# Kernel optimization log

Hardware: AMD Instinct MI355X
Metric: run time of the kernel (lower is better)

Reference implementation:

```python
import jax, jax.numpy as jnp
import numpy as np

B, S, D, H, HD = 1, 4096, 1024, 16, 64
HALF = HD // 2


def setup_inputs() -> dict:
    key = jax.random.key(0)
    ks = jax.random.split(key, 8)
    std = 0.02
    x = jax.random.normal(ks[0], (B, S, D), dtype=jnp.float32)
    wq_w = jax.random.normal(ks[1], (D, D), dtype=jnp.float32) * std
    wk_w = jax.random.normal(ks[2], (D, D), dtype=jnp.float32) * std
    wv_w = jax.random.normal(ks[3], (D, D), dtype=jnp.float32) * std
    wo_w = jax.random.normal(ks[4], (D, D), dtype=jnp.float32) * std
    wq_b = jnp.zeros((D,), jnp.float32)
    wk_b = jnp.zeros((D,), jnp.float32)
    wv_b = jnp.zeros((D,), jnp.float32)
    wo_b = jnp.zeros((D,), jnp.float32)
    # LLaMA-style rotary frequencies: theta = 10000^{-2i/HD}
    inv_freq = 1.0 / (10000.0 ** (jnp.arange(0, HD, 2, dtype=jnp.float32) / HD))  # [HALF]
    t = jnp.arange(S, dtype=jnp.float32)
    angles = jnp.outer(t, inv_freq)  # [S, HALF]
    freqs_cos = jnp.cos(angles)
    freqs_sin = jnp.sin(angles)
    # causal additive mask (finite large-negative to stay grad-safe)
    mask = jnp.triu(jnp.full((S, S), -1e9, dtype=jnp.float32), k=1)[None, None]
    return {
        "x": x, "start_pos": 0, "freqs_cos": freqs_cos, "freqs_sin": freqs_sin,
        "mask": mask,
        "wq_w": wq_w, "wq_b": wq_b, "wk_w": wk_w, "wk_b": wk_b,
        "wv_w": wv_w, "wv_b": wv_b, "wo_w": wo_w, "wo_b": wo_b,
    }


def _apply_rope(t, cos, sin):
    # t: [B, S, H, HD]; cos/sin: [S, HALF]. Complex multiply on consecutive pairs.
    b, s, h, hd = t.shape
    t2 = t.reshape(b, s, h, hd // 2, 2)
    x0, x1 = t2[..., 0], t2[..., 1]
    c = cos[None, :, None, :]
    sn = sin[None, :, None, :]
    o0 = x0 * c - x1 * sn
    o1 = x0 * sn + x1 * c
    return jnp.stack([o0, o1], axis=-1).reshape(b, s, h, hd)


def reference(x, start_pos, freqs_cos, freqs_sin, mask,
              wq_w, wq_b, wk_w, wk_b, wv_w, wv_b, wo_w, wo_b):
    bsz, seqlen, dim = x.shape
    q = (x @ wq_w.T + wq_b).reshape(bsz, seqlen, H, HD)
    k = (x @ wk_w.T + wk_b).reshape(bsz, seqlen, H, HD)
    v = (x @ wv_w.T + wv_b).reshape(bsz, seqlen, H, HD)
    q = _apply_rope(q, freqs_cos, freqs_sin)
    k = _apply_rope(k, freqs_cos, freqs_sin)
    # [B, H, S, HD]
    q = q.transpose(0, 2, 1, 3)
    k = k.transpose(0, 2, 1, 3)
    v = v.transpose(0, 2, 1, 3)
    scores = jnp.einsum('bhqd,bhkd->bhqk', q, k) / jnp.sqrt(jnp.float32(HD))
    scores = scores + mask
    probs = jax.nn.softmax(scores.astype(jnp.float32), axis=-1).astype(q.dtype)
    out = jnp.einsum('bhqk,bhkd->bhqd', probs, v)  # [B, H, S, HD]
    out = out.transpose(0, 2, 1, 3).reshape(bsz, seqlen, dim)
    return out @ wo_w.T + wo_b
```

## Files before the change

### kernel.cpp

```cpp
#include <hip/hip_runtime.h>


#define S_LEN 4096
#define DIM   1024
#define NH    16
#define HD    64

typedef __attribute__((ext_vector_type(8))) short bf16x8;
typedef __attribute__((ext_vector_type(4))) float f32x4;

__device__ __forceinline__ unsigned short f2b(float f) {
  union { float f; unsigned int u; } v; v.f = f;
  unsigned int r = (v.u + 0x7fffu + ((v.u >> 16) & 1u)) >> 16;
  return (unsigned short)r;
}
__device__ __forceinline__ float b2f(unsigned short h) {
  union { unsigned int u; float f; } v; v.u = ((unsigned int)h) << 16;
  return v.f;
}
__device__ __forceinline__ unsigned int pk2t(float a, float b) {
  union { float f; unsigned int u; } x, y; x.f = a; y.f = b;
  return (x.u >> 16) | (y.u & 0xffff0000u);
}
__device__ __forceinline__ void gload16(const void* g, void* l) {
  __builtin_amdgcn_global_load_lds(
      (const __attribute__((address_space(1))) unsigned int*)g,
      (__attribute__((address_space(3))) unsigned int*)l, 16, 0, 0);
}
__device__ __forceinline__ f32x4 fzero4() { f32x4 z = {0.f, 0.f, 0.f, 0.f}; return z; }

__global__ void cvt_all(const float* __restrict__ x, const float* __restrict__ wq,
                        const float* __restrict__ wk, const float* __restrict__ wv,
                        const float* __restrict__ wo, const float* __restrict__ qb,
                        const float* __restrict__ kb, const float* __restrict__ vbs,
                        const float* __restrict__ ob, unsigned short* __restrict__ xb,
                        unsigned short* __restrict__ wqkvb, unsigned short* __restrict__ wobb,
                        float* __restrict__ biasq, float* __restrict__ biaso) {
  int i = blockIdx.x * 256 + threadIdx.x;
  if (i < 2097152) {
    const float* src; unsigned short* dst; int off;
    if (i < 1048576)      { src = x;  dst = xb;              off = i; }
    else if (i < 1310720) { src = wq; dst = wqkvb;           off = i - 1048576; }
    else if (i < 1572864) { src = wk; dst = wqkvb + 1048576; off = i - 1310720; }
    else if (i < 1835008) { src = wv; dst = wqkvb + 2097152; off = i - 1572864; }
    else                  { src = wo; dst = wobb;            off = i - 1835008; }
    float4 v = ((const float4*)src)[off];
    unsigned int lo = (unsigned int)f2b(v.x) | ((unsigned int)f2b(v.y) << 16);
    unsigned int hi = (unsigned int)f2b(v.z) | ((unsigned int)f2b(v.w) << 16);
    ((uint2*)dst)[off] = make_uint2(lo, hi);
  } else if (i < 2097152 + 1024) {
    int j = i - 2097152;
    if (j < 256)      ((float4*)biasq)[j]              = ((const float4*)qb)[j];
    else if (j < 512) ((float4*)(biasq + 1024))[j-256] = ((const float4*)kb)[j-256];
    else if (j < 768) ((float4*)(biasq + 2048))[j-512] = ((const float4*)vbs)[j-512];
    else              ((float4*)biaso)[j-768]          = ((const float4*)ob)[j-768];
  }
}

__global__ __launch_bounds__(256) void gemm_nt(
    const unsigned short* __restrict__ A, const unsigned short* __restrict__ B,
    const float* __restrict__ bias, float* __restrict__ outF,
    unsigned short* __restrict__ dq, unsigned short* __restrict__ dk,
    unsigned short* __restrict__ vtout, const float* __restrict__ fc,
    const float* __restrict__ fs, int M, int N, int K, int mode) {
  __shared__ alignas(16) unsigned short sA[2][128 * 32];
  __shared__ alignas(16) unsigned short sB[2][128 * 32];
  const int tid = threadIdx.x;
  const int lane = tid & 63, wave = tid >> 6;
  const int ln = lane & 15, quad = lane >> 4;
  const int bm = blockIdx.x * 128, bn = blockIdx.y * 128;
  const int wr = (wave >> 1) * 64, wc = (wave & 1) * 64;

  f32x4 acc[4][4];
#pragma unroll
  for (int i = 0; i < 4; ++i)
#pragma unroll
    for (int j = 0; j < 4; ++j) acc[i][j] = fzero4();

#pragma unroll
  for (int i = 0; i < 2; ++i) {
    int o = (i * 256 + tid) * 16;
    int e = o >> 1;
    int row = e >> 5, col = e & 31;
    gload16(A + (size_t)(bm + row) * K + col, (char*)sA[0] + o);
    gload16(B + (size_t)(bn + row) * K + col, (char*)sB[0] + o);
  }

  int buf = 0;
  for (int k0 = 0; k0 < K; k0 += 32, buf ^= 1) {
    __syncthreads();
    if (k0 + 32 < K) {
#pragma unroll
      for (int i = 0; i < 2; ++i) {
        int o = (i * 256 + tid) * 16;
        int e = o >> 1;
        int row = e >> 5, col = e & 31;
        gload16(A + (size_t)(bm + row) * K + k0 + 32 + col, (char*)sA[buf ^ 1] + o);
        gload16(B + (size_t)(bn + row) * K + k0 + 32 + col, (char*)sB[buf ^ 1] + o);
      }
    }
    bf16x8 af[4], bfr[4];
#pragma unroll
    for (int i = 0; i < 4; ++i) {
      af[i]  = *(const bf16x8*)&sA[buf][(wr + i * 16 + ln) * 32 + quad * 8];
      bfr[i] = *(const bf16x8*)&sB[buf][(wc + i * 16 + ln) * 32 + quad * 8];
    }
#pragma unroll
    for (int i = 0; i < 4; ++i)
#pragma unroll
      for (int j = 0; j < 4; ++j)
        acc[i][j] = __builtin_amdgcn_mfma_f32_16x16x32_bf16(af[i], bfr[j], acc[i][j], 0, 0, 0);
  }

  if (mode == 1) {
#pragma unroll
    for (int i = 0; i < 4; ++i)
#pragma unroll
      for (int j = 0; j < 4; ++j) {
        int n = bn + wc + j * 16 + ln;
        float bi = bias[n];
#pragma unroll
        for (int r = 0; r < 4; ++r) {
          int m = bm + wr + i * 16 + quad * 4 + r;
          outF[(size_t)m * N + n] = acc[i][j][r] + bi;
        }
      }
  } else {
    const int bufi = bn >> 10;
    const int hq = ((bn & 1023) + wc) >> 6;
    if (bufi < 2) {
      unsigned short* const base = bufi == 0 ? dq : dk;
      const float qsc = bufi == 0 ? 0.180336880f : 1.0f;
#pragma unroll
      for (int i = 0; i < 4; ++i)
#pragma unroll
        for (int j = 0; j < 4; ++j) {
          int n = bn + wc + j * 16 + ln;
          float bi = bias[n];
          int hd = j * 16 + ln;
          int pi = hd >> 1;
          bool evn = (ln & 1) == 0;
#pragma unroll
          for (int r = 0; r < 4; ++r) {
            int m = bm + wr + i * 16 + quad * 4 + r;
            float val = acc[i][j][r] + bi;
            float par = __shfl_xor(val, 1);
            float c = fc[m * 32 + pi], sn = fs[m * 32 + pi];
            float o = evn ? (val * c - par * sn) : (par * sn + val * c);
            base[((size_t)(hq * S_LEN + m)) * HD + hd] = f2b(o * qsc);
          }
        }
    } else {
      __syncthreads();
      unsigned short* scr =
          (wave < 2 ? (unsigned short*)sA : (unsigned short*)sB) + (wave & 1) * 4096;
#pragma unroll
      for (int i = 0; i < 4; ++i)
#pragma unroll
        for (int j = 0; j < 4; ++j) {
          int n = bn + wc + j * 16 + ln;
          float bi = bias[n];
          int hd = j * 16 + ln;
#pragma unroll
          for (int r = 0; r < 4; ++r) {
            int sl = i * 16 + quad * 4 + r;
            int byte = hd * 128 + ((((sl >> 3) ^ (hd & 7)) << 4)) + (sl & 7) * 2;
            *(unsigned short*)((char*)scr + byte) = f2b(acc[i][j][r] + bi);
          }
        }
#pragma unroll
      for (int pass = 0; pass < 4; ++pass) {
        int row = pass * 16 + ln;
        uint4 d0 = *(uint4*)((char*)scr + row * 128 + (((quad * 2) ^ (row & 7)) << 4));
        uint4 d1 = *(uint4*)((char*)scr + row * 128 + (((quad * 2 + 1) ^ (row & 7)) << 4));
        uint4* dst = (uint4*)(vtout + ((size_t)(hq * HD + row)) * S_LEN + bm + wr + quad * 16);
        dst[0] = d0;
        dst[1] = d1;
      }
    }
  }
}

__device__ __forceinline__ bf16x8 lds_swzK(const unsigned short* s, int row, int chunk) {
  int byte = row * 128 + ((chunk ^ ((row >> 2) & 7)) << 4);
  return *(const bf16x8*)((const char*)s + byte);
}
__device__ __forceinline__ bf16x8 lds_swzV(const unsigned short* s, int row, int chunk) {
  int byte = row * 128 + ((chunk ^ (row & 7)) << 4);
  return *(const bf16x8*)((const char*)s + byte);
}

__global__ __launch_bounds__(256, 4) void flash_kernel(
    const unsigned short* __restrict__ qg, const unsigned short* __restrict__ kg,
    const unsigned short* __restrict__ vtg, unsigned short* __restrict__ attn) {
  __shared__ alignas(16) unsigned short sK[64 * 64];
  __shared__ alignas(16) unsigned short sV[64 * 64];
  __shared__ alignas(16) unsigned short sP[4 * 16 * 72];

  const int tid = threadIdx.x;
  const int lane = tid & 63, wave = tid >> 6;
  const int ln = lane & 15, quad = lane >> 4;
  const int h = blockIdx.y;

  const unsigned short* qh = qg + (size_t)h * (S_LEN * HD);
  const unsigned short* kh = kg + (size_t)h * (S_LEN * HD);
  const unsigned short* vh = vtg + (size_t)h * (HD * S_LEN);

  bf16x8 ones;
#pragma unroll
  for (int j = 0; j < 8; ++j) ones[j] = (short)0x3F80;
  unsigned short* pw = &sP[wave * (16 * 72)];

  for (int p = 0; p < 2; ++p) {
    const int qb = p == 0 ? (int)blockIdx.x : 63 - (int)blockIdx.x;
    const int q0 = qb * 64;
    const int qrow = q0 + wave * 16;

    bf16x8 qf[2];
    qf[0] = *(const bf16x8*)(qh + (size_t)(qrow + ln) * HD + quad * 8);
    qf[1] = *(const bf16x8*)(qh + (size_t)(qrow + ln) * HD + 32 + quad * 8);

    f32x4 o_acc[4];
    f32x4 l_acc = fzero4();
#pragma unroll
    for (int t = 0; t < 4; ++t) o_acc[t] = fzero4();

    const int nkv = qb + 1;
    for (int kt = 0; kt < nkv; ++kt) {
      const int kv0 = kt * 64;
      __syncthreads();
#pragma unroll
      for (int i = 0; i < 2; ++i) {
        int ob = (i * 256 + tid) * 16;
        int row = ob >> 7;
        int ch = (ob >> 4) & 7;
        gload16(kh + (size_t)(kv0 + row) * HD + ((ch ^ ((row >> 2) & 7)) << 3), (char*)sK + ob);
        gload16(vh + (size_t)row * S_LEN + kv0 + ((ch ^ (row & 7)) << 3), (char*)sV + ob);
      }
      __syncthreads();

      f32x4 sc[4];
#pragma unroll
      for (int t = 0; t < 4; ++t) sc[t] = fzero4();
#pragma unroll
      for (int t = 0; t < 4; ++t) {
        int krow = ln * 4 + t;
        bf16x8 kb0 = lds_swzK(sK, krow, quad);
        bf16x8 kb1 = lds_swzK(sK, krow, 4 + quad);
        sc[t] = __builtin_amdgcn_mfma_f32_16x16x32_bf16(qf[0], kb0, sc[t], 0, 0, 0);
        sc[t] = __builtin_amdgcn_mfma_f32_16x16x32_bf16(qf[1], kb1, sc[t], 0, 0, 0);
      }

      if (kt == nkv - 1) {
#pragma unroll
        for (int r = 0; r < 4; ++r) {
          int row = qrow + quad * 4 + r;
          int colb = kv0 + ln * 4;
          float p0 = (colb + 0 <= row) ? __builtin_amdgcn_exp2f(sc[0][r]) : 0.0f;
          float p1 = (colb + 1 <= row) ? __builtin_amdgcn_exp2f(sc[1][r]) : 0.0f;
          float p2 = (colb + 2 <= row) ? __builtin_amdgcn_exp2f(sc[2][r]) : 0.0f;
          float p3 = (colb + 3 <= row) ? __builtin_amdgcn_exp2f(sc[3][r]) : 0.0f;
          *(uint2*)&pw[(quad * 4 + r) * 72 + ln * 4] = make_uint2(pk2t(p0, p1), pk2t(p2, p3));
        }
      } else {
#pragma unroll
        for (int r = 0; r < 4; ++r) {
          float p0 = __builtin_amdgcn_exp2f(sc[0][r]);
          float p1 = __builtin_amdgcn_exp2f(sc[1][r]);
          float p2 = __builtin_amdgcn_exp2f(sc[2][r]);
          float p3 = __builtin_amdgcn_exp2f(sc[3][r]);
          *(uint2*)&pw[(quad * 4 + r) * 72 + ln * 4] = make_uint2(pk2t(p0, p1), pk2t(p2, p3));
        }
      }

      bf16x8 pa0 = *(const bf16x8*)&pw[ln * 72 + quad * 8];
      bf16x8 pa1 = *(const bf16x8*)&pw[ln * 72 + 32 + quad * 8];

      l_acc = __builtin_amdgcn_mfma_f32_16x16x32_bf16(pa0, ones, l_acc, 0, 0, 0);
      l_acc = __builtin_amdgcn_mfma_f32_16x16x32_bf16(pa1, ones, l_acc, 0, 0, 0);

#pragma unroll
      for (int t = 0; t < 4; ++t) {
        int vrow = t * 16 + ln;
        bf16x8 vb0 = lds_swzV(sV, vrow, quad);
        bf16x8 vb1 = lds_swzV(sV, vrow, 4 + quad);
        o_acc[t] = __builtin_amdgcn_mfma_f32_16x16x32_bf16(pa0, vb0, o_acc[t], 0, 0, 0);
        o_acc[t] = __builtin_amdgcn_mfma_f32_16x16x32_bf16(pa1, vb1, o_acc[t], 0, 0, 0);
      }
    }

    float inv[4];
#pragma unroll
    for (int r = 0; r < 4; ++r) inv[r] = 1.0f / l_acc[r];
#pragma unroll
    for (int t = 0; t < 4; ++t)
#pragma unroll
      for (int r = 0; r < 4; ++r) {
        int row = qrow + quad * 4 + r;
        attn[(size_t)row * DIM + h * HD + t * 16 + ln] = f2b(o_acc[t][r] * inv[r]);
      }
  }
}

extern "C" void kernel_launch(void* const* d_in, const int* in_sizes, int n_in,
                              void* d_out, int out_size, void* d_ws, size_t ws_size,
                              hipStream_t stream) {
  const float* x    = (const float*)d_in[0];
  const float* fc   = (const float*)d_in[2];
  const float* fs   = (const float*)d_in[3];
  const float* wqw  = (const float*)d_in[5];
  const float* wqb  = (const float*)d_in[6];
  const float* wkw  = (const float*)d_in[7];
  const float* wkb  = (const float*)d_in[8];
  const float* wvw  = (const float*)d_in[9];
  const float* wvb  = (const float*)d_in[10];
  const float* wow  = (const float*)d_in[11];
  const float* wobf = (const float*)d_in[12];
  float* out = (float*)d_out;

  char* ws = (char*)d_ws;
  const size_t MB = (size_t)1 << 20;
  unsigned short* xb    = (unsigned short*)(ws + 0);
  unsigned short* wqkvb = (unsigned short*)(ws + 8 * MB);
  unsigned short* wobb  = (unsigned short*)(ws + 16 * MB);
  float* biasq = (float*)(ws + 18 * MB);
  float* biaso = (float*)(ws + 18 * MB + 65536);
  unsigned short* qb_ = (unsigned short*)(ws + 19 * MB);
  unsigned short* kb_ = (unsigned short*)(ws + 27 * MB);
  unsigned short* vt  = (unsigned short*)(ws + 35 * MB);
  unsigned short* attn = (unsigned short*)(ws + 0);

  cvt_all<<<8196, 256, 0, stream>>>(x, wqw, wkw, wvw, wow, wqb, wkb, wvb, wobf,
                                    xb, wqkvb, wobb, biasq, biaso);
  gemm_nt<<<dim3(32, 24), 256, 0, stream>>>(xb, wqkvb, biasq, nullptr, qb_, kb_, vt,
                                            fc, fs, 4096, 3072, 1024, 0);
  flash_kernel<<<dim3(32, 16), 256, 0, stream>>>(qb_, kb_, vt, attn);
  gemm_nt<<<dim3(32, 8), 256, 0, stream>>>(attn, wobb, biaso, out, nullptr, nullptr, nullptr,
                                           nullptr, nullptr, 4096, 1024, 1024, 1);
}
```

Baseline: 283.3 us.

## Double-buffer flash K/V tiles, remap heads to blocks, split output GEMM tiles

The flash attention kernel now double-buffers its K and V tiles in shared memory, issuing the next tile's loads before computing the current one and dropping one barrier per iteration. Its grid becomes 1D with a permuted head/query-block mapping, likely aimed at better spreading or cache locality across compute units. The output projection moves to a dedicated kernel with 128x64 tiles, doubling the block count to 512 for better CU occupancy. The trade-off is more LDS per flash block, which may lower occupancy under the 4-blocks launch bound.

```diff
diff --git a/kernel.cpp b/kernel.cpp
--- a/kernel.cpp
+++ b/kernel.cpp
@@ -57,12 +57,11 @@
   }
 }
 
-__global__ __launch_bounds__(256) void gemm_nt(
+__global__ __launch_bounds__(256) void gemm_qkv(
     const unsigned short* __restrict__ A, const unsigned short* __restrict__ B,
-    const float* __restrict__ bias, float* __restrict__ outF,
-    unsigned short* __restrict__ dq, unsigned short* __restrict__ dk,
-    unsigned short* __restrict__ vtout, const float* __restrict__ fc,
-    const float* __restrict__ fs, int M, int N, int K, int mode) {
+    const float* __restrict__ bias, unsigned short* __restrict__ dq,
+    unsigned short* __restrict__ dk, unsigned short* __restrict__ vtout,
+    const float* __restrict__ fc, const float* __restrict__ fs, int K) {
   __shared__ alignas(16) unsigned short sA[2][128 * 32];
   __shared__ alignas(16) unsigned short sB[2][128 * 32];
   const int tid = threadIdx.x;
@@ -112,73 +111,133 @@
         acc[i][j] = __builtin_amdgcn_mfma_f32_16x16x32_bf16(af[i], bfr[j], acc[i][j], 0, 0, 0);
   }
 
-  if (mode == 1) {
+  const int bufi = bn >> 10;
+  const int hq = ((bn & 1023) + wc) >> 6;
+  if (bufi < 2) {
+    unsigned short* const base = bufi == 0 ? dq : dk;
+    const float qsc = bufi == 0 ? 0.180336880f : 1.0f;
 #pragma unroll
     for (int i = 0; i < 4; ++i)
 #pragma unroll
       for (int j = 0; j < 4; ++j) {
         int n = bn + wc + j * 16 + ln;
         float bi = bias[n];
+        int hd = j * 16 + ln;
+        int pi = hd >> 1;
+        bool evn = (ln & 1) == 0;
 #pragma unroll
         for (int r = 0; r < 4; ++r) {
           int m = bm + wr + i * 16 + quad * 4 + r;
-          outF[(size_t)m * N + n] = acc[i][j][r] + bi;
+          float val = acc[i][j][r] + bi;
+          float par = __shfl_xor(val, 1);
+          float c = fc[m * 32 + pi], sn = fs[m * 32 + pi];
+          float o = evn ? (val * c - par * sn) : (par * sn + val * c);
+          base[((size_t)(hq * S_LEN + m)) * HD + hd] = f2b(o * qsc);
         }
       }
   } else {
-    const int bufi = bn >> 10;
-    const int hq = ((bn & 1023) + wc) >> 6;
-    if (bufi < 2) {
-      unsigned short* const base = bufi == 0 ? dq : dk;
-      const float qsc = bufi == 0 ? 0.180336880f : 1.0f;
-#pragma unroll
-      for (int i = 0; i < 4; ++i)
-#pragma unroll
-        for (int j = 0; j < 4; ++j) {
-          int n = bn + wc + j * 16 + ln;
-          float bi = bias[n];
-          int hd = j * 16 + ln;
-          int pi = hd >> 1;
-          bool evn = (ln & 1) == 0;
-#pragma unroll
-          for (int r = 0; r < 4; ++r) {
-            int m = bm + wr + i * 16 + quad * 4 + r;
-            float val = acc[i][j][r] + bi;
-            float par = __shfl_xor(val, 1);
-            float c = fc[m * 32 + pi], sn = fs[m * 32 + pi];
-            float o = evn ? (val * c - par * sn) : (par * sn + val * c);
-            base[((size_t)(hq * S_LEN + m)) * HD + hd] = f2b(o * qsc);
-          }
+    __syncthreads();
+    unsigned short* scr =
+        (wave < 2 ? (unsigned short*)sA : (unsigned short*)sB) + (wave & 1) * 4096;
+#pragma unroll
+    for (int i = 0; i < 4; ++i)
+#pragma unroll
+      for (int j = 0; j < 4; ++j) {
+        int n = bn + wc + j * 16 + ln;
+        float bi = bias[n];
+        int hd = j * 16 + ln;
+#pragma unroll
+        for (int r = 0; r < 4; ++r) {
+          int sl = i * 16 + quad * 4 + r;
+          int byte = hd * 128 + ((((sl >> 3) ^ (hd & 7)) << 4)) + (sl & 7) * 2;
+          *(unsigned short*)((char*)scr + byte) = f2b(acc[i][j][r] + bi);
         }
-    } else {
-      __syncthreads();
-      unsigned short* scr =
-          (wave < 2 ? (unsigned short*)sA : (unsigned short*)sB) + (wave & 1) * 4096;
-#pragma unroll
-      for (int i = 0; i < 4; ++i)
-#pragma unroll
-        for (int j = 0; j < 4; ++j) {
-          int n = bn + wc + j * 16 + ln;
-          float bi = bias[n];
-          int hd = j * 16 + ln;
-#pragma unroll
-          for (int r = 0; r < 4; ++r) {
-            int sl = i * 16 + quad * 4 + r;
-            int byte = hd * 128 + ((((sl >> 3) ^ (hd & 7)) << 4)) + (sl & 7) * 2;
-            *(unsigned short*)((char*)scr + byte) = f2b(acc[i][j][r] + bi);
-          }
-        }
-#pragma unroll
-      for (int pass = 0; pass < 4; ++pass) {
-        int row = pass * 16 + ln;
-        uint4 d0 = *(uint4*)((char*)scr + row * 128 + (((quad * 2) ^ (row & 7)) << 4));
-        uint4 d1 = *(uint4*)((char*)scr + row * 128 + (((quad * 2 + 1) ^ (row & 7)) << 4));
-        uint4* dst = (uint4*)(vtout + ((size_t)(hq * HD + row)) * S_LEN + bm + wr + quad * 16);
-        dst[0] = d0;
-        dst[1] = d1;
-      }
-    }
-  }
+      }
+#pragma unroll
+    for (int pass = 0; pass < 4; ++pass) {
+      int row = pass * 16 + ln;
+      uint4 d0 = *(uint4*)((char*)scr + row * 128 + (((quad * 2) ^ (row & 7)) << 4));
+      uint4 d1 = *(uint4*)((char*)scr + row * 128 + (((quad * 2 + 1) ^ (row & 7)) << 4));
+      uint4* dst = (uint4*)(vtout + ((size_t)(hq * HD + row)) * S_LEN + bm + wr + quad * 16);
+      dst[0] = d0;
+      dst[1] = d1;
+    }
+  }
+}
+
+__global__ __launch_bounds__(256) void gemm_out(
+    const unsigned short* __restrict__ A, const unsigned short* __restrict__ B,
+    const float* __restrict__ bias, float* __restrict__ outF, int N, int K) {
+  __shared__ alignas(16) unsigned short sA[2][128 * 32];
+  __shared__ alignas(16) unsigned short sB[2][64 * 32];
+  const int tid = threadIdx.x;
+  const int lane = tid & 63, wave = tid >> 6;
+  const int ln = lane & 15, quad = lane >> 4;
+  const int bm = blockIdx.x * 128, bn = blockIdx.y * 64;
+  const int wr = (wave >> 1) * 64, wc = (wave & 1) * 32;
+
+  f32x4 acc[4][2];
+#pragma unroll
+  for (int i = 0; i < 4; ++i)
+#pragma unroll
+    for (int j = 0; j < 2; ++j) acc[i][j] = fzero4();
+
+  {
+#pragma unroll
+    for (int i = 0; i < 2; ++i) {
+      int o = (i * 256 + tid) * 16;
+      int e = o >> 1;
+      int row = e >> 5, col = e & 31;
+      gload16(A + (size_t)(bm + row) * K + col, (char*)sA[0] + o);
+    }
+    int o = tid * 16;
+    int e = o >> 1;
+    int row = e >> 5, col = e & 31;
+    gload16(B + (size_t)(bn + row) * K + col, (char*)sB[0] + o);
+  }
+
+  int buf = 0;
+  for (int k0 = 0; k0 < K; k0 += 32, buf ^= 1) {
+    __syncthreads();
+    if (k0 + 32 < K) {
+#pragma unroll
+      for (int i = 0; i < 2; ++i) {
+        int o = (i * 256 + tid) * 16;
+        int e = o >> 1;
+        int row = e >> 5, col = e & 31;
+        gload16(A + (size_t)(bm + row) * K + k0 + 32 + col, (char*)sA[buf ^ 1] + o);
+      }
+      int o = tid * 16;
+      int e = o >> 1;
+      int row = e >> 5, col = e & 31;
+      gload16(B + (size_t)(bn + row) * K + k0 + 32 + col, (char*)sB[buf ^ 1] + o);
+    }
+    bf16x8 af[4], bfr[2];
+#pragma unroll
+    for (int i = 0; i < 4; ++i)
+      af[i] = *(const bf16x8*)&sA[buf][(wr + i * 16 + ln) * 32 + quad * 8];
+#pragma unroll
+    for (int j = 0; j < 2; ++j)
+      bfr[j] = *(const bf16x8*)&sB[buf][(wc + j * 16 + ln) * 32 + quad * 8];
+#pragma unroll
+    for (int i = 0; i < 4; ++i)
+#pragma unroll
+      for (int j = 0; j < 2; ++j)
+        acc[i][j] = __builtin_amdgcn_mfma_f32_16x16x32_bf16(af[i], bfr[j], acc[i][j], 0, 0, 0);
+  }
+
+#pragma unroll
+  for (int i = 0; i < 4; ++i)
+#pragma unroll
+    for (int j = 0; j < 2; ++j) {
+      int n = bn + wc + j * 16 + ln;
+      float bi = bias[n];
+#pragma unroll
+      for (int r = 0; r < 4; ++r) {
+        int m = bm + wr + i * 16 + quad * 4 + r;
+        outF[(size_t)m * N + n] = acc[i][j][r] + bi;
+      }
+    }
 }
 
 __device__ __forceinline__ bf16x8 lds_swzK(const unsigned short* s, int row, int chunk) {
@@ -193,14 +252,16 @@
 __global__ __launch_bounds__(256, 4) void flash_kernel(
     const unsigned short* __restrict__ qg, const unsigned short* __restrict__ kg,
     const unsigned short* __restrict__ vtg, unsigned short* __restrict__ attn) {
-  __shared__ alignas(16) unsigned short sK[64 * 64];
-  __shared__ alignas(16) unsigned short sV[64 * 64];
+  __shared__ alignas(16) unsigned short sK[2][64 * 64];
+  __shared__ alignas(16) unsigned short sV[2][64 * 64];
   __shared__ alignas(16) unsigned short sP[4 * 16 * 72];
 
   const int tid = threadIdx.x;
   const int lane = tid & 63, wave = tid >> 6;
   const int ln = lane & 15, quad = lane >> 4;
-  const int h = blockIdx.y;
+  const int c = blockIdx.x;
+  const int h = 2 * (c & 7) + ((c >> 3) & 1);
+  const int xp = c >> 4;
 
   const unsigned short* qh = qg + (size_t)h * (S_LEN * HD);
   const unsigned short* kh = kg + (size_t)h * (S_LEN * HD);
@@ -212,7 +273,7 @@
   unsigned short* pw = &sP[wave * (16 * 72)];
 
   for (int p = 0; p < 2; ++p) {
-    const int qb = p == 0 ? (int)blockIdx.x : 63 - (int)blockIdx.x;
+    const int qb = p == 0 ? xp : 63 - xp;
     const int q0 = qb * 64;
     const int qrow = q0 + wave * 16;
 
@@ -226,27 +287,45 @@
     for (int t = 0; t < 4; ++t) o_acc[t] = fzero4();
 
     const int nkv = qb + 1;
-    for (int kt = 0; kt < nkv; ++kt) {
+
+    __syncthreads();
+#pragma unroll
+    for (int i = 0; i < 2; ++i) {
+      int ob = (i * 256 + tid) * 16;
+      int row = ob >> 7;
+      int ch = (ob >> 4) & 7;
+      gload16(kh + (size_t)row * HD + ((ch ^ ((row >> 2) & 7)) << 3), (char*)sK[0] + ob);
+      gload16(vh + (size_t)row * S_LEN + ((ch ^ (row & 7)) << 3), (char*)sV[0] + ob);
+    }
+
+    int buf = 0;
+    for (int kt = 0; kt < nkv; ++kt, buf ^= 1) {
       const int kv0 = kt * 64;
       __syncthreads();
-#pragma unroll
-      for (int i = 0; i < 2; ++i) {
-        int ob = (i * 256 + tid) * 16;
-        int row = ob >> 7;
-        int ch = (ob >> 4) & 7;
-        gload16(kh + (size_t)(kv0 + row) * HD + ((ch ^ ((row >> 2) & 7)) << 3), (char*)sK + ob);
-        gload16(vh + (size_t)row * S_LEN + kv0 + ((ch ^ (row & 7)) << 3), (char*)sV + ob);
-      }
-      __syncthreads();
-
+      if (kt + 1 < nkv) {
+        const int kv1 = kv0 + 64;
+#pragma unroll
+        for (int i = 0; i < 2; ++i) {
+          int ob = (i * 256 + tid) * 16;
+          int row = ob >> 7;
+          int ch = (ob >> 4) & 7;
+          gload16(kh + (size_t)(kv1 + row) * HD + ((ch ^ ((row >> 2) & 7)) << 3),
+                  (char*)sK[buf ^ 1] + ob);
+          gload16(vh + (size_t)row * S_LEN + kv1 + ((ch ^ (row & 7)) << 3),
+                  (char*)sV[buf ^ 1] + ob);
+        }
+      }
+
+      const unsigned short* kp = sK[buf];
+      const unsigned short* vp = sV[buf];
       f32x4 sc[4];
 #pragma unroll
       for (int t = 0; t < 4; ++t) sc[t] = fzero4();
 #pragma unroll
       for (int t = 0; t < 4; ++t) {
         int krow = ln * 4 + t;
-        bf16x8 kb0 = lds_swzK(sK, krow, quad);
-        bf16x8 kb1 = lds_swzK(sK, krow, 4 + quad);
+        bf16x8 kb0 = lds_swzK(kp, krow, quad);
+        bf16x8 kb1 = lds_swzK(kp, krow, 4 + quad);
         sc[t] = __builtin_amdgcn_mfma_f32_16x16x32_bf16(qf[0], kb0, sc[t], 0, 0, 0);
         sc[t] = __builtin_amdgcn_mfma_f32_16x16x32_bf16(qf[1], kb1, sc[t], 0, 0, 0);
       }
@@ -282,8 +361,8 @@
 #pragma unroll
       for (int t = 0; t < 4; ++t) {
         int vrow = t * 16 + ln;
-        bf16x8 vb0 = lds_swzV(sV, vrow, quad);
-        bf16x8 vb1 = lds_swzV(sV, vrow, 4 + quad);
+        bf16x8 vb0 = lds_swzV(vp, vrow, quad);
+        bf16x8 vb1 = lds_swzV(vp, vrow, 4 + quad);
         o_acc[t] = __builtin_amdgcn_mfma_f32_16x16x32_bf16(pa0, vb0, o_acc[t], 0, 0, 0);
         o_acc[t] = __builtin_amdgcn_mfma_f32_16x16x32_bf16(pa1, vb1, o_acc[t], 0, 0, 0);
       }
@@ -332,9 +411,7 @@
 
   cvt_all<<<8196, 256, 0, stream>>>(x, wqw, wkw, wvw, wow, wqb, wkb, wvb, wobf,
                                     xb, wqkvb, wobb, biasq, biaso);
-  gemm_nt<<<dim3(32, 24), 256, 0, stream>>>(xb, wqkvb, biasq, nullptr, qb_, kb_, vt,
-                                            fc, fs, 4096, 3072, 1024, 0);
-  flash_kernel<<<dim3(32, 16), 256, 0, stream>>>(qb_, kb_, vt, attn);
-  gemm_nt<<<dim3(32, 8), 256, 0, stream>>>(attn, wobb, biaso, out, nullptr, nullptr, nullptr,
-                                           nullptr, nullptr, 4096, 1024, 1024, 1);
-}
+  gemm_qkv<<<dim3(32, 24), 256, 0, stream>>>(xb, wqkvb, biasq, qb_, kb_, vt, fc, fs, 1024);
+  flash_kernel<<<512, 256, 0, stream>>>(qb_, kb_, vt, attn);
+  gemm_out<<<dim3(32, 16), 256, 0, stream>>>(attn, wobb, biaso, out, 1024, 1024);
+}
```

New measurement: 267.7 us. 5.5% less time.
